# Optimization experiments

Measured on AMD Instinct MI355X. Metric: run time of the kernel, lower is better.

The kernel has to match this reference:

```python
import jax, jax.numpy as jnp
import numpy as np

P, V, D = 1024, 49408, 512


def setup_inputs() -> dict:
    key = jax.random.key(0)
    k1, k2 = jax.random.split(key)
    prompt_embs = jax.random.normal(k1, (P, D), dtype=jnp.float32)
    clip_embs = jax.random.normal(k2, (V, D), dtype=jnp.float32)
    return {"prompt_embs": prompt_embs, "clip_embs": clip_embs}


def reference(prompt_embs, clip_embs):
    # torch.cdist(p=2): Euclidean distance matrix [P, V].
    # ||a-b||^2 = ||a||^2 + ||b||^2 - 2 a.b ; sqrt is monotone so argmin of
    # the (clamped) squared distance matches argmin of the true distance.
    a2 = jnp.sum(prompt_embs * prompt_embs, axis=-1, keepdims=True)   # [P,1]
    b2 = jnp.sum(clip_embs * clip_embs, axis=-1)                      # [V]
    ab = jnp.einsum("pd,vd->pv", prompt_embs, clip_embs)              # [P,V]
    d2 = jnp.maximum(a2 + b2[None, :] - 2.0 * ab, 0.0)                # [P,V]
    prompt_ids = jnp.argmin(d2, axis=1)                               # [P]
    new_embs = clip_embs[prompt_ids]                                  # [P,D] gather
    return new_embs, prompt_ids
```

## Files before the change

kernel.cpp:

```cpp
#include <hip/hip_runtime.h>
#include <stdint.h>

#define NP 1024
#define NV 49408
#define ND 512
#define NTILE 48

typedef __attribute__((ext_vector_type(8))) __bf16 bf16x8;
typedef __attribute__((ext_vector_type(4))) float f32x4;
typedef __attribute__((ext_vector_type(4))) int i32x4;

__device__ inline unsigned long long pack_sv(float s, unsigned v) {
  unsigned u = __float_as_uint(s);
  u = (u & 0x80000000u) ? ~u : (u | 0x80000000u);
  return ((unsigned long long)u << 32) | (unsigned long long)v;
}

__global__ __launch_bounds__(256) void pack_a_k(const float* __restrict__ src,
                                                __bf16* __restrict__ dst) {
  int lane = threadIdx.x & 63;
  int row = blockIdx.x * 4 + (threadIdx.x >> 6);
  const float* r = src + (size_t)row * ND + lane * 8;
  float4 x0 = *(const float4*)r;
  float4 x1 = *(const float4*)(r + 4);
  float xs[8] = {x0.x, x0.y, x0.z, x0.w, x1.x, x1.y, x1.z, x1.w};
  bf16x8 hi, lo;
#pragma unroll
  for (int j = 0; j < 8; ++j) {
    float x = xs[j];
    __bf16 h = (__bf16)x;
    hi[j] = h;
    lo[j] = (__bf16)(x - (float)h);
  }
  const int mb = row >> 4, rr = row & 15;
  const int tHi = lane >> 2, g = lane & 3;
  size_t cHi = (((size_t)tHi * 64) + mb) * 64 + g * 16 + rr;
  size_t cLo = (((size_t)(tHi + 16) * 64) + mb) * 64 + g * 16 + rr;
  *(bf16x8*)(dst + cHi * 8) = hi;
  *(bf16x8*)(dst + cLo * 8) = lo;
}

__global__ __launch_bounds__(256) void pack_b_k(const float* __restrict__ src,
                                                __bf16* __restrict__ dst,
                                                float* __restrict__ sumsq) {
  int lane = threadIdx.x & 63;
  int row = blockIdx.x * 4 + (threadIdx.x >> 6);
  const float* r = src + (size_t)row * ND + lane * 8;
  float4 x0 = *(const float4*)r;
  float4 x1 = *(const float4*)(r + 4);
  float xs[8] = {x0.x, x0.y, x0.z, x0.w, x1.x, x1.y, x1.z, x1.w};
  bf16x8 hi, lo;
  float ss = 0.f;
#pragma unroll
  for (int j = 0; j < 8; ++j) {
    float x = xs[j];
    ss += x * x;
    __bf16 h = (__bf16)x;
    hi[j] = h;
    lo[j] = (__bf16)(x - (float)h);
  }
  __bf16* drow = dst + (size_t)row * 1024 + lane * 8;
  *(bf16x8*)drow = hi;
  *(bf16x8*)(drow + 512) = lo;
#pragma unroll
  for (int m = 1; m < 64; m <<= 1) ss += __shfl_xor(ss, m);
  if (lane == 0) sumsq[row] = ss;
}


__device__ __attribute__((always_inline)) static inline
void gll16(const char* src, char* dst) {
  __builtin_amdgcn_global_load_lds(
      (const __attribute__((address_space(1))) void*)src,
      (__attribute__((address_space(3))) void*)dst, 16, 0, 0);
}

__device__ __attribute__((always_inline)) static inline
bf16x8 lds_read(unsigned addr) {
  i32x4 d;
  asm volatile("ds_read_b128 %0, %1" : "=v"(d) : "v"(addr));
  return __builtin_bit_cast(bf16x8, d);
}

#define FENCE asm volatile("" ::: "memory")

__device__ __attribute__((always_inline)) static inline
int bByte(int t) {
  int tt = (t < NTILE) ? t : t - NTILE;
  return (tt & 15) * 64 + (tt >= 32 ? 1024 : 0);
}

template <int J>
__device__ __attribute__((always_inline)) static inline
void phase_op(f32x4 (&acc)[4][4], bf16x8 (&aE)[4], bf16x8 (&aO)[4],
              bf16x8 (&bE)[4], bf16x8 (&bO)[4],
              const char* Ab, const int (&voffA)[4],
              const char* srcBt, char* stB, unsigned bRead, int p) {
  constexpr int RS = (J + 3) & 3;
  constexpr int RR = (J + 1) & 3;
  const int kB = bByte(p + 3);
  const int kA = ((p + 1) & 31) * 65536;
  bf16x8 (&aN)[4] = (J % 2 == 0) ? aO : aE;
  bf16x8 (&aC)[4] = (J % 2 == 0) ? aE : aO;
  bf16x8 (&bN)[4] = (J % 2 == 0) ? bO : bE;
  bf16x8 (&bC)[4] = (J % 2 == 0) ? bE : bO;
  gll16(srcBt + kB, stB + RS * 8192);
  gll16(srcBt + kB + 131072, stB + RS * 8192 + 4096);
#pragma unroll
  for (int m = 0; m < 4; ++m)
    aN[m] = *(const bf16x8*)(Ab + voffA[m] + kA);
#pragma unroll
  for (int n = 0; n < 4; ++n)
    bN[n] = lds_read(bRead + RR * 8192 + n * 1024);
  asm volatile("s_waitcnt vmcnt(6) lgkmcnt(4)" ::: "memory");
  __builtin_amdgcn_sched_barrier(0);
  __builtin_amdgcn_s_setprio(1);
#pragma unroll
  for (int m = 0; m < 4; ++m)
#pragma unroll
    for (int n = 0; n < 4; ++n)
      acc[m][n] = __builtin_amdgcn_mfma_f32_16x16x32_bf16(aC[m], bC[n], acc[m][n], 0, 0, 0);
  __builtin_amdgcn_s_setprio(0);
  FENCE;
  __builtin_amdgcn_s_barrier();
  FENCE;
}

__global__ __launch_bounds__(256, 3) void gemm_argmin_k(const __bf16* __restrict__ A,
                                                        const __bf16* __restrict__ B,
                                                        const float* __restrict__ b2,
                                                        unsigned long long* __restrict__ best) {
  __shared__ __align__(16) char lds[32768];
  const int tid = threadIdx.x;
  const int lane = tid & 63;
  const int wid = tid >> 6;
  const int wm = wid >> 1;
  const int wn = wid & 1;

  const int d = blockIdx.x;
  const int o = (d & 7) * 386 + (d >> 3);
  const int bm = (o & 7) * 128;
  const int bn = (o >> 3) * 128;

  const int r = lane & 15, g = lane >> 4;
  const int rh = r >> 1;
  const unsigned lds0 =
      (unsigned)(uintptr_t)(const __attribute__((address_space(3))) char*)(const char*)lds;
  const unsigned bRead = lds0 + wn * 4096 + rh * 128 + (r & 1) * 64 + (((g + rh) & 3) << 4);

  const char* Ab = (const char*)A;
  int voffA[4];
#pragma unroll
  for (int m = 0; m < 4; ++m)
    voffA[m] = ((bm >> 4) + wm * 4 + m) * 1024 + lane * 16;

  const int srow = 2 * (tid >> 3) + ((tid >> 2) & 1);
  const int sc16 = ((tid & 3) - (tid >> 3)) & 3;
  const char* srcBt = (const char*)B + (size_t)(bn + srow) * 2048 + sc16 * 16;
  char* stB = (char*)lds + tid * 16;

  f32x4 acc[4][4] = {};
  bf16x8 aE[4], aO[4], bE[4], bO[4];

  gll16(srcBt + bByte(0), stB + 0);
  gll16(srcBt + bByte(0) + 131072, stB + 4096);
  gll16(srcBt + bByte(1), stB + 8192);
  gll16(srcBt + bByte(1) + 131072, stB + 8192 + 4096);
  gll16(srcBt + bByte(2), stB + 16384);
  gll16(srcBt + bByte(2) + 131072, stB + 16384 + 4096);
#pragma unroll
  for (int m = 0; m < 4; ++m)
    aE[m] = *(const bf16x8*)(Ab + voffA[m]);
  asm volatile("s_waitcnt vmcnt(6)" ::: "memory");
  FENCE;
  __builtin_amdgcn_s_barrier();
  FENCE;
#pragma unroll
  for (int n = 0; n < 4; ++n)
    bE[n] = lds_read(bRead + n * 1024);

#pragma unroll 1
  for (int it = 0; it < 12; ++it) {
    const int p0 = 4 * it;
    phase_op<0>(acc, aE, aO, bE, bO, Ab, voffA, srcBt, stB, bRead, p0 + 0);
    phase_op<1>(acc, aE, aO, bE, bO, Ab, voffA, srcBt, stB, bRead, p0 + 1);
    phase_op<2>(acc, aE, aO, bE, bO, Ab, voffA, srcBt, stB, bRead, p0 + 2);
    phase_op<3>(acc, aE, aO, bE, bO, Ab, voffA, srcBt, stB, bRead, p0 + 3);
  }

  float bb[4];
#pragma unroll
  for (int n = 0; n < 4; ++n) bb[n] = b2[bn + wn * 64 + n * 16 + r];
#pragma unroll
  for (int m = 0; m < 4; ++m) {
#pragma unroll
    for (int reg = 0; reg < 4; ++reg) {
      unsigned long long pk = ~0ull;
#pragma unroll
      for (int n = 0; n < 4; ++n) {
        float s = bb[n] - 2.0f * acc[m][n][reg];
        unsigned long long cand = pack_sv(s, (unsigned)(bn + wn * 64 + n * 16 + r));
        pk = (cand < pk) ? cand : pk;
      }
#pragma unroll
      for (int msk = 1; msk < 16; msk <<= 1) {
        unsigned long long o2 = __shfl_xor(pk, msk);
        pk = (o2 < pk) ? o2 : pk;
      }
      if (r == 0) atomicMin(&best[bm + wm * 64 + m * 16 + g * 4 + reg], pk);
    }
  }
}

__global__ __launch_bounds__(256) void naive_argmin_k(const float* __restrict__ A,
                                                      const float* __restrict__ B,
                                                      unsigned long long* __restrict__ best) {
  __shared__ float arow[ND];
  int p = blockIdx.y;
  unsigned v = blockIdx.x * 256 + threadIdx.x;
  for (int i = threadIdx.x; i < ND; i += 256) arow[i] = A[(size_t)p * ND + i];
  __syncthreads();
  const float4* br = (const float4*)(B + (size_t)v * ND);
  float s = 0.f;
#pragma unroll 4
  for (int i = 0; i < ND / 4; ++i) {
    float4 b = br[i];
    const float4 a = *(const float4*)&arow[i * 4];
    float d0 = a.x - b.x, d1 = a.y - b.y, d2 = a.z - b.z, d3 = a.w - b.w;
    s += d0 * d0 + d1 * d1 + d2 * d2 + d3 * d3;
  }
  unsigned long long pk = pack_sv(s, v);
#pragma unroll
  for (int msk = 1; msk < 64; msk <<= 1) {
    unsigned long long o = __shfl_xor(pk, msk);
    pk = (o < pk) ? o : pk;
  }
  if ((threadIdx.x & 63) == 0) atomicMin(&best[p], pk);
}

__global__ __launch_bounds__(128) void gather_k(const unsigned long long* __restrict__ best,
                                                const float* __restrict__ clip,
                                                float* __restrict__ out) {
  int p = blockIdx.x;
  unsigned long long pk = best[p];
  unsigned v = (unsigned)(pk & 0xffffffffull);
  const float4* src = (const float4*)(clip + (size_t)v * ND);
  float4* dst = (float4*)(out + (size_t)p * ND);
  dst[threadIdx.x] = src[threadIdx.x];
  if (threadIdx.x == 0) out[(size_t)NP * ND + p] = (float)v;
}

extern "C" void kernel_launch(void* const* d_in, const int* in_sizes, int n_in,
                              void* d_out, int out_size, void* d_ws, size_t ws_size,
                              hipStream_t stream) {
  const float* prompt = (const float*)d_in[0];
  const float* clip = (const float*)d_in[1];
  float* out = (float*)d_out;

  size_t off = 0;
  unsigned long long* best = (unsigned long long*)d_ws;
  off += (size_t)NP * 8;
  float* b2 = (float*)((char*)d_ws + off);
  off += (size_t)NV * 4;
  off = (off + 255) & ~(size_t)255;
  __bf16* Ap = (__bf16*)((char*)d_ws + off);
  off += (size_t)NP * 1024 * 2;
  __bf16* Bp = (__bf16*)((char*)d_ws + off);
  off += (size_t)NV * 1024 * 2;
  const size_t need = off;

  if (ws_size >= need) {
    hipMemsetAsync(best, 0xFF, (size_t)NP * 8, stream);
    pack_a_k<<<NP / 4, 256, 0, stream>>>(prompt, Ap);
    pack_b_k<<<NV / 4, 256, 0, stream>>>(clip, Bp, b2);
    gemm_argmin_k<<<dim3(8 * 386), 256, 0, stream>>>(Ap, Bp, b2, best);
    gather_k<<<NP, 128, 0, stream>>>(best, clip, out);
  } else {
    hipMemsetAsync(best, 0xFF, (size_t)NP * 8, stream);
    dim3 grid(NV / 256, NP);
    naive_argmin_k<<<grid, 256, 0, stream>>>(prompt, clip, best);
    gather_k<<<NP, 128, 0, stream>>>(best, clip, out);
  }
}
```

Before: 222.7 us.

## Process two K-tiles per barrier with six-slot LDS ring

Restructures the GEMM main loop so each phase consumes two K tiles between barriers, using a 6-stage LDS ring (48KB) instead of 4 stages (32KB). B fragments are read from LDS just in time, and A register prefetch is interleaved between the two MFMA groups. This halves the number of workgroup barriers and deepens the global prefetch, at the cost of more LDS per block, which may reduce occupancy from the requested 3 blocks per CU.

```diff
diff --git a/kernel.cpp b/kernel.cpp
--- a/kernel.cpp
+++ b/kernel.cpp
@@ -93,34 +93,46 @@
 template <int J>
 __device__ __attribute__((always_inline)) static inline
 void phase_op(f32x4 (&acc)[4][4], bf16x8 (&aE)[4], bf16x8 (&aO)[4],
-              bf16x8 (&bE)[4], bf16x8 (&bO)[4],
               const char* Ab, const int (&voffA)[4],
               const char* srcBt, char* stB, unsigned bRead, int p) {
-  constexpr int RS = (J + 3) & 3;
-  constexpr int RR = (J + 1) & 3;
-  const int kB = bByte(p + 3);
-  const int kA = ((p + 1) & 31) * 65536;
-  bf16x8 (&aN)[4] = (J % 2 == 0) ? aO : aE;
-  bf16x8 (&aC)[4] = (J % 2 == 0) ? aE : aO;
-  bf16x8 (&bN)[4] = (J % 2 == 0) ? bO : bE;
-  bf16x8 (&bC)[4] = (J % 2 == 0) ? bE : bO;
-  gll16(srcBt + kB, stB + RS * 8192);
-  gll16(srcBt + kB + 131072, stB + RS * 8192 + 4096);
-#pragma unroll
-  for (int m = 0; m < 4; ++m)
-    aN[m] = *(const bf16x8*)(Ab + voffA[m] + kA);
-#pragma unroll
-  for (int n = 0; n < 4; ++n)
-    bN[n] = lds_read(bRead + RR * 8192 + n * 1024);
-  asm volatile("s_waitcnt vmcnt(6) lgkmcnt(4)" ::: "memory");
+  constexpr int R0 = 2 * J, R1 = 2 * J + 1;
+  constexpr int S0 = (2 * J + 4) % 6, S1 = (2 * J + 5) % 6;
+  const int kB0 = bByte(2 * p + 4), kB1 = bByte(2 * p + 5);
+  const int kAE = ((2 * p + 2) & 31) * 65536;
+  const int kAO = ((2 * p + 3) & 31) * 65536;
+  gll16(srcBt + kB0, stB + S0 * 8192);
+  gll16(srcBt + kB0 + 131072, stB + S0 * 8192 + 4096);
+  gll16(srcBt + kB1, stB + S1 * 8192);
+  gll16(srcBt + kB1 + 131072, stB + S1 * 8192 + 4096);
+  bf16x8 b0[4], b1[4];
+#pragma unroll
+  for (int n = 0; n < 4; ++n) b0[n] = lds_read(bRead + R0 * 8192 + n * 1024);
+#pragma unroll
+  for (int n = 0; n < 4; ++n) b1[n] = lds_read(bRead + R1 * 8192 + n * 1024);
+  asm volatile("s_waitcnt vmcnt(8) lgkmcnt(4)" ::: "memory");
   __builtin_amdgcn_sched_barrier(0);
   __builtin_amdgcn_s_setprio(1);
 #pragma unroll
   for (int m = 0; m < 4; ++m)
 #pragma unroll
     for (int n = 0; n < 4; ++n)
-      acc[m][n] = __builtin_amdgcn_mfma_f32_16x16x32_bf16(aC[m], bC[n], acc[m][n], 0, 0, 0);
+      acc[m][n] = __builtin_amdgcn_mfma_f32_16x16x32_bf16(aE[m], b0[n], acc[m][n], 0, 0, 0);
   __builtin_amdgcn_s_setprio(0);
+#pragma unroll
+  for (int m = 0; m < 4; ++m)
+    aE[m] = *(const bf16x8*)(Ab + voffA[m] + kAE);
+  asm volatile("s_waitcnt vmcnt(8) lgkmcnt(0)" ::: "memory");
+  __builtin_amdgcn_sched_barrier(0);
+  __builtin_amdgcn_s_setprio(1);
+#pragma unroll
+  for (int m = 0; m < 4; ++m)
+#pragma unroll
+    for (int n = 0; n < 4; ++n)
+      acc[m][n] = __builtin_amdgcn_mfma_f32_16x16x32_bf16(aO[m], b1[n], acc[m][n], 0, 0, 0);
+  __builtin_amdgcn_s_setprio(0);
+#pragma unroll
+  for (int m = 0; m < 4; ++m)
+    aO[m] = *(const bf16x8*)(Ab + voffA[m] + kAO);
   FENCE;
   __builtin_amdgcn_s_barrier();
   FENCE;
@@ -130,7 +142,7 @@
                                                         const __bf16* __restrict__ B,
                                                         const float* __restrict__ b2,
                                                         unsigned long long* __restrict__ best) {
-  __shared__ __align__(16) char lds[32768];
+  __shared__ __align__(16) char lds[49152];
   const int tid = threadIdx.x;
   const int lane = tid & 63;
   const int wid = tid >> 6;
@@ -160,7 +172,7 @@
   char* stB = (char*)lds + tid * 16;
 
   f32x4 acc[4][4] = {};
-  bf16x8 aE[4], aO[4], bE[4], bO[4];
+  bf16x8 aE[4], aO[4];
 
   gll16(srcBt + bByte(0), stB + 0);
   gll16(srcBt + bByte(0) + 131072, stB + 4096);
@@ -168,24 +180,25 @@
   gll16(srcBt + bByte(1) + 131072, stB + 8192 + 4096);
   gll16(srcBt + bByte(2), stB + 16384);
   gll16(srcBt + bByte(2) + 131072, stB + 16384 + 4096);
+  gll16(srcBt + bByte(3), stB + 24576);
+  gll16(srcBt + bByte(3) + 131072, stB + 24576 + 4096);
 #pragma unroll
   for (int m = 0; m < 4; ++m)
     aE[m] = *(const bf16x8*)(Ab + voffA[m]);
-  asm volatile("s_waitcnt vmcnt(6)" ::: "memory");
+#pragma unroll
+  for (int m = 0; m < 4; ++m)
+    aO[m] = *(const bf16x8*)(Ab + voffA[m] + 65536);
+  asm volatile("s_waitcnt vmcnt(12)" ::: "memory");
   FENCE;
   __builtin_amdgcn_s_barrier();
   FENCE;
-#pragma unroll
-  for (int n = 0; n < 4; ++n)
-    bE[n] = lds_read(bRead + n * 1024);
 
 #pragma unroll 1
-  for (int it = 0; it < 12; ++it) {
-    const int p0 = 4 * it;
-    phase_op<0>(acc, aE, aO, bE, bO, Ab, voffA, srcBt, stB, bRead, p0 + 0);
-    phase_op<1>(acc, aE, aO, bE, bO, Ab, voffA, srcBt, stB, bRead, p0 + 1);
-    phase_op<2>(acc, aE, aO, bE, bO, Ab, voffA, srcBt, stB, bRead, p0 + 2);
-    phase_op<3>(acc, aE, aO, bE, bO, Ab, voffA, srcBt, stB, bRead, p0 + 3);
+  for (int it = 0; it < 8; ++it) {
+    const int p0 = 3 * it;
+    phase_op<0>(acc, aE, aO, Ab, voffA, srcBt, stB, bRead, p0 + 0);
+    phase_op<1>(acc, aE, aO, Ab, voffA, srcBt, stB, bRead, p0 + 1);
+    phase_op<2>(acc, aE, aO, Ab, voffA, srcBt, stB, bRead, p0 + 2);
   }
 
   float bb[4];
```

Result: faster. 213.2 us, median of 2 (-4.3%).

## Pre-swizzle B into MFMA fragment layout and load directly from global

Applied to the files above, without the earlier changes.

The B-matrix packing kernel now writes clip embeddings in a tiled, MFMA-fragment-ordered layout, matching what A already uses. The GEMM then loads B fragments straight from global memory into registers with register double-buffering, instead of staging through LDS with global_load_lds, ds_read and per-phase barriers. This drops the LDS traffic and block-wide synchronisation. In exchange, each wave fetches its own B fragments with no sharing across the two wm waves, which raises global/L2 traffic and exposes latency without the deeper prefetch.

```diff
diff --git a/kernel.cpp b/kernel.cpp
--- a/kernel.cpp
+++ b/kernel.cpp
@@ -5,10 +5,10 @@
 #define NV 49408
 #define ND 512
 #define NTILE 48
+#define BSTRIDE 3162112
 
 typedef __attribute__((ext_vector_type(8))) __bf16 bf16x8;
 typedef __attribute__((ext_vector_type(4))) float f32x4;
-typedef __attribute__((ext_vector_type(4))) int i32x4;
 
 __device__ inline unsigned long long pack_sv(float s, unsigned v) {
   unsigned u = __float_as_uint(s);
@@ -59,35 +59,24 @@
     hi[j] = h;
     lo[j] = (__bf16)(x - (float)h);
   }
-  __bf16* drow = dst + (size_t)row * 1024 + lane * 8;
-  *(bf16x8*)drow = hi;
-  *(bf16x8*)(drow + 512) = lo;
+  const int nb = row >> 4, rr = row & 15;
+  const int tHi = lane >> 2, g = lane & 3;
+  size_t cHi = (((size_t)tHi * 3088) + nb) * 64 + g * 16 + rr;
+  size_t cLo = (((size_t)(tHi + 16) * 3088) + nb) * 64 + g * 16 + rr;
+  *(bf16x8*)(dst + cHi * 8) = hi;
+  *(bf16x8*)(dst + cLo * 8) = lo;
 #pragma unroll
   for (int m = 1; m < 64; m <<= 1) ss += __shfl_xor(ss, m);
   if (lane == 0) sumsq[row] = ss;
 }
 
 
+#define FENCE asm volatile("" ::: "memory")
+
 __device__ __attribute__((always_inline)) static inline
-void gll16(const char* src, char* dst) {
-  __builtin_amdgcn_global_load_lds(
-      (const __attribute__((address_space(1))) void*)src,
-      (__attribute__((address_space(3))) void*)dst, 16, 0, 0);
-}
-
-__device__ __attribute__((always_inline)) static inline
-bf16x8 lds_read(unsigned addr) {
-  i32x4 d;
-  asm volatile("ds_read_b128 %0, %1" : "=v"(d) : "v"(addr));
-  return __builtin_bit_cast(bf16x8, d);
-}
-
-#define FENCE asm volatile("" ::: "memory")
-
-__device__ __attribute__((always_inline)) static inline
-int bByte(int t) {
+int bTileByte(int t) {
   int tt = (t < NTILE) ? t : t - NTILE;
-  return (tt & 15) * 64 + (tt >= 32 ? 1024 : 0);
+  return ((tt & 15) + (tt >= 32 ? 16 : 0)) * BSTRIDE;
 }
 
 template <int J>
@@ -95,25 +84,19 @@
 void phase_op(f32x4 (&acc)[4][4], bf16x8 (&aE)[4], bf16x8 (&aO)[4],
               bf16x8 (&bE)[4], bf16x8 (&bO)[4],
               const char* Ab, const int (&voffA)[4],
-              const char* srcBt, char* stB, unsigned bRead, int p) {
-  constexpr int RS = (J + 3) & 3;
-  constexpr int RR = (J + 1) & 3;
-  const int kB = bByte(p + 3);
-  const int kA = ((p + 1) & 31) * 65536;
-  bf16x8 (&aN)[4] = (J % 2 == 0) ? aO : aE;
-  bf16x8 (&aC)[4] = (J % 2 == 0) ? aE : aO;
-  bf16x8 (&bN)[4] = (J % 2 == 0) ? bO : bE;
-  bf16x8 (&bC)[4] = (J % 2 == 0) ? bE : bO;
-  gll16(srcBt + kB, stB + RS * 8192);
-  gll16(srcBt + kB + 131072, stB + RS * 8192 + 4096);
+              const char* Bb, const int (&voffB)[4], int t) {
+  const int kA = ((t + 1) & 31) * 65536;
+  const int kB = bTileByte(t + 1);
+  bf16x8 (&aN)[4] = (J == 0) ? aO : aE;
+  bf16x8 (&aC)[4] = (J == 0) ? aE : aO;
+  bf16x8 (&bN)[4] = (J == 0) ? bO : bE;
+  bf16x8 (&bC)[4] = (J == 0) ? bE : bO;
 #pragma unroll
   for (int m = 0; m < 4; ++m)
     aN[m] = *(const bf16x8*)(Ab + voffA[m] + kA);
 #pragma unroll
   for (int n = 0; n < 4; ++n)
-    bN[n] = lds_read(bRead + RR * 8192 + n * 1024);
-  asm volatile("s_waitcnt vmcnt(6) lgkmcnt(4)" ::: "memory");
-  __builtin_amdgcn_sched_barrier(0);
+    bN[n] = *(const bf16x8*)(Bb + voffB[n] + kB);
   __builtin_amdgcn_s_setprio(1);
 #pragma unroll
   for (int m = 0; m < 4; ++m)
@@ -121,16 +104,12 @@
     for (int n = 0; n < 4; ++n)
       acc[m][n] = __builtin_amdgcn_mfma_f32_16x16x32_bf16(aC[m], bC[n], acc[m][n], 0, 0, 0);
   __builtin_amdgcn_s_setprio(0);
-  FENCE;
-  __builtin_amdgcn_s_barrier();
-  FENCE;
 }
 
 __global__ __launch_bounds__(256, 3) void gemm_argmin_k(const __bf16* __restrict__ A,
                                                         const __bf16* __restrict__ B,
                                                         const float* __restrict__ b2,
                                                         unsigned long long* __restrict__ best) {
-  __shared__ __align__(16) char lds[32768];
   const int tid = threadIdx.x;
   const int lane = tid & 63;
   const int wid = tid >> 6;
@@ -143,51 +122,35 @@
   const int bn = (o >> 3) * 128;
 
   const int r = lane & 15, g = lane >> 4;
-  const int rh = r >> 1;
-  const unsigned lds0 =
-      (unsigned)(uintptr_t)(const __attribute__((address_space(3))) char*)(const char*)lds;
-  const unsigned bRead = lds0 + wn * 4096 + rh * 128 + (r & 1) * 64 + (((g + rh) & 3) << 4);
+  (void)g;
 
   const char* Ab = (const char*)A;
-  int voffA[4];
+  const char* Bb = (const char*)B;
+  int voffA[4], voffB[4];
 #pragma unroll
   for (int m = 0; m < 4; ++m)
     voffA[m] = ((bm >> 4) + wm * 4 + m) * 1024 + lane * 16;
-
-  const int srow = 2 * (tid >> 3) + ((tid >> 2) & 1);
-  const int sc16 = ((tid & 3) - (tid >> 3)) & 3;
-  const char* srcBt = (const char*)B + (size_t)(bn + srow) * 2048 + sc16 * 16;
-  char* stB = (char*)lds + tid * 16;
+#pragma unroll
+  for (int n = 0; n < 4; ++n)
+    voffB[n] = ((bn >> 4) + wn * 4 + n) * 1024 + lane * 16;
 
   f32x4 acc[4][4] = {};
   bf16x8 aE[4], aO[4], bE[4], bO[4];
 
-  gll16(srcBt + bByte(0), stB + 0);
-  gll16(srcBt + bByte(0) + 131072, stB + 4096);
-  gll16(srcBt + bByte(1), stB + 8192);
-  gll16(srcBt + bByte(1) + 131072, stB + 8192 + 4096);
-  gll16(srcBt + bByte(2), stB + 16384);
-  gll16(srcBt + bByte(2) + 131072, stB + 16384 + 4096);
 #pragma unroll
   for (int m = 0; m < 4; ++m)
     aE[m] = *(const bf16x8*)(Ab + voffA[m]);
-  asm volatile("s_waitcnt vmcnt(6)" ::: "memory");
-  FENCE;
-  __builtin_amdgcn_s_barrier();
-  FENCE;
 #pragma unroll
   for (int n = 0; n < 4; ++n)
-    bE[n] = lds_read(bRead + n * 1024);
+    bE[n] = *(const bf16x8*)(Bb + voffB[n]);
 
 #pragma unroll 1
-  for (int it = 0; it < 12; ++it) {
-    const int p0 = 4 * it;
-    phase_op<0>(acc, aE, aO, bE, bO, Ab, voffA, srcBt, stB, bRead, p0 + 0);
-    phase_op<1>(acc, aE, aO, bE, bO, Ab, voffA, srcBt, stB, bRead, p0 + 1);
-    phase_op<2>(acc, aE, aO, bE, bO, Ab, voffA, srcBt, stB, bRead, p0 + 2);
-    phase_op<3>(acc, aE, aO, bE, bO, Ab, voffA, srcBt, stB, bRead, p0 + 3);
-  }
-
+  for (int it = 0; it < NTILE / 2; ++it) {
+    phase_op<0>(acc, aE, aO, bE, bO, Ab, voffA, Bb, voffB, 2 * it);
+    phase_op<1>(acc, aE, aO, bE, bO, Ab, voffA, Bb, voffB, 2 * it + 1);
+  }
+
+  const int gg = lane >> 4;
   float bb[4];
 #pragma unroll
   for (int n = 0; n < 4; ++n) bb[n] = b2[bn + wn * 64 + n * 16 + r];
@@ -207,7 +170,7 @@
         unsigned long long o2 = __shfl_xor(pk, msk);
         pk = (o2 < pk) ? o2 : pk;
       }
-      if (r == 0) atomicMin(&best[bm + wm * 64 + m * 16 + g * 4 + reg], pk);
+      if (r == 0) atomicMin(&best[bm + wm * 64 + m * 16 + gg * 4 + reg], pk);
     }
   }
 }
```

Result: slower. 245.5 us (+10.3%).
